# Performance work log

Measured on AMD Instinct MI355X. Metric: run time of the kernel, lower is better.

Reference implementation:

```python
import jax, jax.numpy as jnp
import numpy as np

KINEMATIC_CHAIN = [[0, 2, 5, 8, 11], [0, 1, 4, 7, 10], [0, 3, 6, 9, 12, 15],
                   [9, 14, 17, 19, 21], [9, 13, 16, 18, 20]]
PATHS = [c[1:] for c in KINEMATIC_CHAIN]  # paths = chain[1:] per gauss_integral_motion
FRAMES, JOINTS = 16384, 22


def setup_inputs() -> dict:
    key = jax.random.key(0)
    k1, k2 = jax.random.split(key)
    motion1 = jax.random.normal(k1, (FRAMES, JOINTS, 3), dtype=jnp.float32)
    motion2 = jax.random.normal(k2, (FRAMES, JOINTS, 3), dtype=jnp.float32)
    return {"motion1": motion1, "motion2": motion2}


def _safe_normalize(v):
    # vec / norm(vec) if norm != 0 else zeros  (matches the torch list comp)
    n = jnp.linalg.norm(v, axis=-1, keepdims=True)
    return jnp.where(n > 0, v / jnp.where(n > 0, n, 1.0), 0.0)


def _gli_pair(p1, p2):
    """Sum of Gauss link integrals over all segment pairs of two paths.
    p1: (L1, 3), p2: (L2, 3) -> scalar. Vectorized over the (L1-1, L2-1) segment grid."""
    s1, e1 = p1[:-1, None, :], p1[1:, None, :]   # (n1, 1, 3)
    s2, e2 = p2[None, :-1, :], p2[None, 1:, :]   # (1, n2, 3)
    r13, r14 = s2 - s1, e2 - s1
    r23, r24 = s2 - e1, e2 - e1
    r12, r34 = e1 - s1, e2 - s2
    faces = [jnp.cross(r13, r14), jnp.cross(r14, r24),
             jnp.cross(r24, r23), jnp.cross(r23, r13)]
    nf = [_safe_normalize(f) for f in faces]
    gli = jnp.zeros(jnp.broadcast_shapes(r13.shape[:-1], r24.shape[:-1]), p1.dtype)
    for i in range(4):
        d = jnp.clip(jnp.sum(nf[i] * nf[(i + 1) % 4], axis=-1), -1.0, 1.0)
        gli = gli + jnp.arcsin(d)
    sign = jnp.sum(jnp.cross(r34, r12) * r13, axis=-1)
    gli = gli * jnp.where(sign > 0, 1.0, -1.0) / (4.0 * jnp.pi)
    return jnp.sum(gli)


def _window_mask(motion1, motion2):
    # xz bounding-box overlap per frame, then dilate each contiguous run by 1
    # frame on each side (start = count-1, end = count+1-1 in the torch code).
    def bbox(m):  # (F, J, 3) -> min/max over joints of x and z
        x, z = m[..., 0], m[..., 2]
        return x.min(1), x.max(1), z.min(1), z.max(1)
    x1n, x1x, z1n, z1x = bbox(motion1)
    x2n, x2x, z2n, z2x = bbox(motion2)
    ov_x = ~((x1x < x2n) | (x2x < x1n))
    ov_z = ~((z1x < z2n) | (z2x < z1n))
    f = ov_x & ov_z  # (F,) bool
    false1 = jnp.zeros((1,), dtype=bool)
    prev = jnp.concatenate([false1, f[:-1]])
    nxt = jnp.concatenate([f[1:], false1])
    return f | prev | nxt


def _gli_motion(motion1, motion2):
    frame = motion1.shape[0]
    n_paths = len(PATHS)
    mask = _window_mask(motion1, motion2).astype(motion1.dtype)  # (F,)
    # GLI_motion[i, a, b]: vmap each path-pair over frames (25 fixed pairs)
    rows = []
    for pa in PATHS:
        p1 = motion1[:, jnp.asarray(pa), :]  # (F, La, 3)
        cols = []
        for pb in PATHS:
            p2 = motion2[:, jnp.asarray(pb), :]  # (F, Lb, 3)
            cols.append(jax.vmap(_gli_pair)(p1, p2))  # (F,)
        rows.append(jnp.stack(cols, axis=-1))  # (F, n_paths)
    gli = jnp.stack(rows, axis=-2)  # (F, n_paths, n_paths)
    gli = gli * mask[:, None, None]  # frames outside windows stay zero
    vel = jnp.abs(gli[1:] - gli[:-1]).reshape(frame - 1, n_paths * n_paths)
    return jnp.max(vel, axis=1)  # (F-1,)


def reference(motion1, motion2):
    return _gli_motion(motion1, motion2)
```

## Files before the change

kernel.cpp:

```cpp
#include <hip/hip_runtime.h>
#include <math.h>

#define NFRAMES 16384
#define NJOINTS 22
#define NPATHS  5
#define NPAIRS  (NPATHS * NPATHS)
#define NSEG    16
#define GSTRIDE 32
#define FSTR    (NJOINTS * 3)

typedef float v2f __attribute__((ext_vector_type(2)));

__constant__ int2 c_seg[NSEG] = {
    {6,15},{15,24},{24,33},
    {3,12},{12,21},{21,30},
    {9,18},{18,27},{27,36},{36,45},
    {42,51},{51,57},{57,63},
    {39,48},{48,54},{54,60}
};
__constant__ int c_pstart[NPATHS] = {0, 3, 6, 10, 13};
__constant__ int c_plen[NPATHS]   = {3, 3, 4, 3, 3};

struct V3 { v2f x, y, z; };
__device__ __forceinline__ V3 vsub(V3 a, V3 b) { V3 r; r.x=a.x-b.x; r.y=a.y-b.y; r.z=a.z-b.z; return r; }
__device__ __forceinline__ v2f vdot(V3 a, V3 b) { return a.x*b.x + a.y*b.y + a.z*b.z; }
__device__ __forceinline__ V3 vcross(V3 a, V3 b) {
    V3 r;
    r.x = a.y*b.z - a.z*b.y;
    r.y = a.z*b.x - a.x*b.z;
    r.z = a.x*b.y - a.y*b.x;
    return r;
}

__device__ __forceinline__ v2f vfast_asin(v2f x) {
    v2f a = __builtin_elementwise_max(x, -x);
    v2f p = a * -0.0187293f + 0.0742610f;
    p = a * p + -0.2121144f;
    p = a * p + 1.5707288f;
    v2f s;
    s.x = __builtin_amdgcn_sqrtf(1.0f - a.x);
    s.y = __builtin_amdgcn_sqrtf(1.0f - a.y);
    v2f r = 1.5707963268f - s * p;
    r.x = (x.x < 0.0f) ? -r.x : r.x;
    r.y = (x.y < 0.0f) ? -r.y : r.y;
    return r;
}

__device__ __forceinline__ v2f vasin_term(v2f d, v2f ma, v2f mb) {
    v2f m = ma * mb;
    v2f rs;
    rs.x = __builtin_amdgcn_rsqf(m.x);
    rs.y = __builtin_amdgcn_rsqf(m.y);
    v2f one = 1.0f, mone = -1.0f;
    v2f x = __builtin_elementwise_min(one, __builtin_elementwise_max(mone, d * rs));
    v2f r = vfast_asin(x);
    r.x = (ma.x > 0.0f && mb.x > 0.0f) ? r.x : 0.0f;
    r.y = (ma.y > 0.0f && mb.y > 0.0f) ? r.y : 0.0f;
    return r;
}

__global__ __launch_bounds__(256) void k_gli(const float* __restrict__ m1,
                                             const float* __restrict__ m2,
                                             float* __restrict__ gli,
                                             int* __restrict__ ov) {
    __shared__ v2f sA[FSTR];
    __shared__ v2f sB[FSTR];
    __shared__ float sT0[257];
    __shared__ float sT1[257];

    int f0 = blockIdx.x * 2;
    int t = threadIdx.x;
    const float* a0 = m1 + (size_t)f0 * FSTR;
    const float* b0 = m2 + (size_t)f0 * FSTR;

    float* sAf = (float*)sA;
    float* sBf = (float*)sB;
    if (t < FSTR)               sAf[2 * t] = a0[t];
    else if (t < 2 * FSTR)      sBf[2 * (t - FSTR)] = b0[t - FSTR];
    else if (t < 3 * FSTR)      sAf[2 * (t - 2 * FSTR) + 1] = a0[FSTR + (t - 2 * FSTR)];
    else                        sBf[2 * (t - 3 * FSTR) + 1] = b0[FSTR + (t - 3 * FSTR)];
    if (t < 8)                  sBf[2 * (58 + t) + 1] = b0[FSTR + 58 + t];
    if (t == 0) { sT0[256] = 0.0f; sT1[256] = 0.0f; }
    __syncthreads();

    int i = t >> 4;
    int j = t & 15;
    int2 o1 = c_seg[i];
    int2 o2 = c_seg[j];
    V3 s1; s1.x = sA[o1.x]; s1.y = sA[o1.x+1]; s1.z = sA[o1.x+2];
    V3 e1; e1.x = sA[o1.y]; e1.y = sA[o1.y+1]; e1.z = sA[o1.y+2];
    V3 s2; s2.x = sB[o2.x]; s2.y = sB[o2.x+1]; s2.z = sB[o2.x+2];
    V3 e2; e2.x = sB[o2.y]; e2.y = sB[o2.y+1]; e2.z = sB[o2.y+2];

    V3 r12 = vsub(e1, s1);
    V3 r13 = vsub(s2, s1);
    V3 r14 = vsub(e2, s1);

    V3 f0v = vcross(r13, r14);
    V3 c1  = vcross(r12, r13);
    V3 c2  = vcross(r12, r14);
    V3 f2  = vsub(vsub(c2, c1), f0v);

    v2f q0 = vdot(f0v, f0v);
    v2f q1 = vdot(c2, c2);
    v2f q2 = vdot(f2, f2);
    v2f q3 = vdot(c1, c1);

    v2f g = vasin_term( vdot(f0v, c2), q0, q1)
          + vasin_term( vdot(c2, f2),  q1, q2)
          + vasin_term(-vdot(f2, c1),  q2, q3)
          + vasin_term(-vdot(c1, f0v), q3, q0);

    v2f sg = -vdot(c2, r13);
    sT0[t] = (sg.x > 0.0f) ? g.x : -g.x;
    sT1[t] = (sg.y > 0.0f) ? g.y : -g.y;

    int w = t >> 6;
    if (w == 1 || w == 2) {
        int fr = w - 1;
        int half = (t >> 5) & 1;
        int jj = t & 31;
        if (jj > NJOINTS - 1) jj = NJOINTS - 1;
        const float* p = (half ? sBf : sAf);
        float x = p[2 * (jj * 3 + 0) + fr];
        float z = p[2 * (jj * 3 + 2) + fr];
        float xn = x, xx = x, zn = z, zx = z;
#pragma unroll
        for (int k = 1; k < 32; k <<= 1) {
            xn = fminf(xn, __shfl_xor(xn, k, 32));
            xx = fmaxf(xx, __shfl_xor(xx, k, 32));
            zn = fminf(zn, __shfl_xor(zn, k, 32));
            zx = fmaxf(zx, __shfl_xor(zx, k, 32));
        }
        float oxn = __shfl_xor(xn, 32, 64);
        float oxx = __shfl_xor(xx, 32, 64);
        float ozn = __shfl_xor(zn, 32, 64);
        float ozx = __shfl_xor(zx, 32, 64);
        if ((t & 63) == 0) {
            bool ovx = !((xx < oxn) || (oxx < xn));
            bool ovz = !((zx < ozn) || (ozx < zn));
            ov[f0 + fr] = (ovx && ovz) ? 1 : 0;
        }
    }
    __syncthreads();

    int tt = -1;
    const float* sT = sT0;
    int fo = f0;
    if (t < NPAIRS) { tt = t; }
    else if (t >= 32 && t < 32 + NPAIRS) { tt = t - 32; sT = sT1; fo = f0 + 1; }
    if (tt >= 0) {
        int pa = (tt * 205) >> 10;
        int pb = tt - pa * 5;
        int ia0 = c_pstart[pa], na = c_plen[pa];
        int ib0 = c_pstart[pb], nb = c_plen[pb];
        float s = 0.0f;
#pragma unroll
        for (int ka = 0; ka < 4; ka++) {
#pragma unroll
            for (int kb = 0; kb < 4; kb++) {
                int idx = (ka < na && kb < nb) ? ((ia0 + ka) * 16 + (ib0 + kb)) : 256;
                s += sT[idx];
            }
        }
        gli[(size_t)fo * GSTRIDE + tt] = s * 0.07957747154594767f;
    }
}

__global__ void k_out(const float* __restrict__ gli, const int* __restrict__ ov,
                      float* __restrict__ out) {
    int f = blockIdx.x * blockDim.x + threadIdx.x;
    if (f >= NFRAMES - 1) return;

    int m0 = ov[f];
    if (f > 0) m0 |= ov[f - 1];
    m0 |= ov[f + 1];

    int m1 = ov[f + 1] | ov[f];
    if (f + 2 <= NFRAMES - 1) m1 |= ov[f + 2];

    float ma = m0 ? 1.0f : 0.0f;
    float mb = m1 ? 1.0f : 0.0f;

    const float4* g0v = (const float4*)(gli + (size_t)f * GSTRIDE);
    const float4* g1v = (const float4*)(gli + (size_t)(f + 1) * GSTRIDE);
    float v = 0.0f;
#pragma unroll
    for (int q = 0; q < 6; q++) {
        float4 u0 = g0v[q];
        float4 u1 = g1v[q];
        v = fmaxf(v, fabsf(u1.x * mb - u0.x * ma));
        v = fmaxf(v, fabsf(u1.y * mb - u0.y * ma));
        v = fmaxf(v, fabsf(u1.z * mb - u0.z * ma));
        v = fmaxf(v, fabsf(u1.w * mb - u0.w * ma));
    }
    {
        float u0 = ((const float*)g0v)[24];
        float u1 = ((const float*)g1v)[24];
        v = fmaxf(v, fabsf(u1 * mb - u0 * ma));
    }
    out[f] = v;
}

extern "C" void kernel_launch(void* const* d_in, const int* in_sizes, int n_in,
                              void* d_out, int out_size, void* d_ws, size_t ws_size,
                              hipStream_t stream) {
    const float* m1 = (const float*)d_in[0];
    const float* m2 = (const float*)d_in[1];
    float* out = (float*)d_out;

    float* gli = (float*)d_ws;
    int* ov = (int*)(gli + (size_t)NFRAMES * GSTRIDE);

    k_gli<<<NFRAMES / 2, 256, 0, stream>>>(m1, m2, gli, ov);

    {
        int threads = 256;
        int blocks = (NFRAMES - 1 + threads - 1) / threads;
        k_out<<<blocks, threads, 0, stream>>>(gli, ov, out);
    }
}
```

Baseline: 80.69 us.

## Give each wavefront its own frame pair, processing 8 frames per block

Restructures k_gli so each of the four wavefronts in a block handles a separate frame pair. Each lane loops over 4 segment pairs, reusing its second-path segment loads across the loop, and every wavefront also does its own bbox overlap reduction using paired (v2f) shuffles. This cuts the block count by four and keeps lanes busy that previously sat idle in the bbox and reduction phases. The cost is more serial work per thread and more shared memory per block, which could lower occupancy or hurt latency hiding. The __syncthreads calls remain block-wide even though the data is now per-wavefront.

```diff
diff --git a/kernel.cpp b/kernel.cpp
--- a/kernel.cpp
+++ b/kernel.cpp
@@ -8,6 +8,7 @@
 #define NSEG    16
 #define GSTRIDE 32
 #define FSTR    (NJOINTS * 3)
+#define FPB     8
 
 typedef float v2f __attribute__((ext_vector_type(2)));
 
@@ -59,111 +60,140 @@
     return r;
 }
 
+__device__ __forceinline__ v2f shfl_xor_v2(v2f v, int mask, int width) {
+    v2f r;
+    r.x = __shfl_xor(v.x, mask, width);
+    r.y = __shfl_xor(v.y, mask, width);
+    return r;
+}
+
 __global__ __launch_bounds__(256) void k_gli(const float* __restrict__ m1,
                                              const float* __restrict__ m2,
                                              float* __restrict__ gli,
                                              int* __restrict__ ov) {
-    __shared__ v2f sA[FSTR];
-    __shared__ v2f sB[FSTR];
-    __shared__ float sT0[257];
-    __shared__ float sT1[257];
-
-    int f0 = blockIdx.x * 2;
+    __shared__ v2f sF[4][2 * FSTR];
+    __shared__ v2f sT[4][260];
+
     int t = threadIdx.x;
-    const float* a0 = m1 + (size_t)f0 * FSTR;
-    const float* b0 = m2 + (size_t)f0 * FSTR;
-
-    float* sAf = (float*)sA;
-    float* sBf = (float*)sB;
-    if (t < FSTR)               sAf[2 * t] = a0[t];
-    else if (t < 2 * FSTR)      sBf[2 * (t - FSTR)] = b0[t - FSTR];
-    else if (t < 3 * FSTR)      sAf[2 * (t - 2 * FSTR) + 1] = a0[FSTR + (t - 2 * FSTR)];
-    else                        sBf[2 * (t - 3 * FSTR) + 1] = b0[FSTR + (t - 3 * FSTR)];
-    if (t < 8)                  sBf[2 * (58 + t) + 1] = b0[FSTR + 58 + t];
-    if (t == 0) { sT0[256] = 0.0f; sT1[256] = 0.0f; }
+    int w = t >> 6;
+    int l = t & 63;
+    int fp = blockIdx.x * FPB + 2 * w;
+    const float* a = m1 + (size_t)fp * FSTR;
+    const float* b = m2 + (size_t)fp * FSTR;
+
+    v2f* sFw = sF[w];
+    float* sFf = (float*)sFw;
+
+    {
+        int u1 = l + 64;
+        int fr1 = (u1 >= FSTR) ? 1 : 0;
+        int co1 = u1 - fr1 * FSTR;
+        float a0v = a[l], a1v = a[u1];
+        float b0v = b[l], b1v = b[u1];
+        sFf[2 * l] = a0v;
+        sFf[2 * co1 + fr1] = a1v;
+        sFf[2 * FSTR + 2 * l] = b0v;
+        sFf[2 * FSTR + 2 * co1 + fr1] = b1v;
+        if (l < 2 * FSTR - 128) {
+            int u2 = l + 128;
+            int co2 = u2 - FSTR;
+            sFf[2 * co2 + 1] = a[u2];
+            sFf[2 * FSTR + 2 * co2 + 1] = b[u2];
+        }
+        if (l == 32) sT[w][256] = v2f{0.0f, 0.0f};
+    }
     __syncthreads();
 
-    int i = t >> 4;
-    int j = t & 15;
-    int2 o1 = c_seg[i];
-    int2 o2 = c_seg[j];
-    V3 s1; s1.x = sA[o1.x]; s1.y = sA[o1.x+1]; s1.z = sA[o1.x+2];
-    V3 e1; e1.x = sA[o1.y]; e1.y = sA[o1.y+1]; e1.z = sA[o1.y+2];
-    V3 s2; s2.x = sB[o2.x]; s2.y = sB[o2.x+1]; s2.z = sB[o2.x+2];
-    V3 e2; e2.x = sB[o2.y]; e2.y = sB[o2.y+1]; e2.z = sB[o2.y+2];
-
-    V3 r12 = vsub(e1, s1);
-    V3 r13 = vsub(s2, s1);
-    V3 r14 = vsub(e2, s1);
-
-    V3 f0v = vcross(r13, r14);
-    V3 c1  = vcross(r12, r13);
-    V3 c2  = vcross(r12, r14);
-    V3 f2  = vsub(vsub(c2, c1), f0v);
-
-    v2f q0 = vdot(f0v, f0v);
-    v2f q1 = vdot(c2, c2);
-    v2f q2 = vdot(f2, f2);
-    v2f q3 = vdot(c1, c1);
-
-    v2f g = vasin_term( vdot(f0v, c2), q0, q1)
-          + vasin_term( vdot(c2, f2),  q1, q2)
-          + vasin_term(-vdot(f2, c1),  q2, q3)
-          + vasin_term(-vdot(c1, f0v), q3, q0);
-
-    v2f sg = -vdot(c2, r13);
-    sT0[t] = (sg.x > 0.0f) ? g.x : -g.x;
-    sT1[t] = (sg.y > 0.0f) ? g.y : -g.y;
-
-    int w = t >> 6;
-    if (w == 1 || w == 2) {
-        int fr = w - 1;
-        int half = (t >> 5) & 1;
-        int jj = t & 31;
+    {
+        int j = l & 15;
+        int i0 = l >> 4;
+        int2 o2 = c_seg[j];
+        const v2f* B = sFw + FSTR;
+        V3 s2; s2.x = B[o2.x]; s2.y = B[o2.x+1]; s2.z = B[o2.x+2];
+        V3 e2; e2.x = B[o2.y]; e2.y = B[o2.y+1]; e2.z = B[o2.y+2];
+        V3 r34 = vsub(e2, s2);
+        for (int k = 0; k < 4; k++) {
+            int2 o1 = c_seg[i0 + 4 * k];
+            V3 s1; s1.x = sFw[o1.x]; s1.y = sFw[o1.x+1]; s1.z = sFw[o1.x+2];
+            V3 e1; e1.x = sFw[o1.y]; e1.y = sFw[o1.y+1]; e1.z = sFw[o1.y+2];
+
+            V3 r12 = vsub(e1, s1);
+            V3 r13 = vsub(s2, s1);
+            V3 r14 = vsub(e2, s1);
+
+            V3 f0v = vcross(r13, r14);
+            V3 c1  = vcross(r12, r13);
+            V3 c2  = vcross(r12, r14);
+            V3 f2  = vsub(vsub(c2, c1), f0v);
+
+            v2f q0 = vdot(f0v, f0v);
+            v2f q1 = vdot(c2, c2);
+            v2f q2 = vdot(f2, f2);
+            v2f q3 = vdot(c1, c1);
+
+            v2f g = vasin_term( vdot(f0v, c2), q0, q1)
+                  + vasin_term( vdot(c2, f2),  q1, q2)
+                  + vasin_term(-vdot(f2, c1),  q2, q3)
+                  + vasin_term(-vdot(c1, f0v), q3, q0);
+
+            v2f sg = -vdot(c2, r13);
+            v2f res;
+            res.x = (sg.x > 0.0f) ? g.x : -g.x;
+            res.y = (sg.y > 0.0f) ? g.y : -g.y;
+            sT[w][l + 64 * k] = res;
+        }
+        (void)r34;
+    }
+
+    {
+        int half = l >> 5;
+        int jj = l & 31;
         if (jj > NJOINTS - 1) jj = NJOINTS - 1;
-        const float* p = (half ? sBf : sAf);
-        float x = p[2 * (jj * 3 + 0) + fr];
-        float z = p[2 * (jj * 3 + 2) + fr];
-        float xn = x, xx = x, zn = z, zx = z;
+        const v2f* p = sFw + half * FSTR;
+        v2f x = p[jj * 3 + 0];
+        v2f z = p[jj * 3 + 2];
+        v2f xn = x, xx = x, zn = z, zx = z;
 #pragma unroll
         for (int k = 1; k < 32; k <<= 1) {
-            xn = fminf(xn, __shfl_xor(xn, k, 32));
-            xx = fmaxf(xx, __shfl_xor(xx, k, 32));
-            zn = fminf(zn, __shfl_xor(zn, k, 32));
-            zx = fmaxf(zx, __shfl_xor(zx, k, 32));
-        }
-        float oxn = __shfl_xor(xn, 32, 64);
-        float oxx = __shfl_xor(xx, 32, 64);
-        float ozn = __shfl_xor(zn, 32, 64);
-        float ozx = __shfl_xor(zx, 32, 64);
-        if ((t & 63) == 0) {
-            bool ovx = !((xx < oxn) || (oxx < xn));
-            bool ovz = !((zx < ozn) || (ozx < zn));
-            ov[f0 + fr] = (ovx && ovz) ? 1 : 0;
+            xn = __builtin_elementwise_min(xn, shfl_xor_v2(xn, k, 32));
+            xx = __builtin_elementwise_max(xx, shfl_xor_v2(xx, k, 32));
+            zn = __builtin_elementwise_min(zn, shfl_xor_v2(zn, k, 32));
+            zx = __builtin_elementwise_max(zx, shfl_xor_v2(zx, k, 32));
+        }
+        v2f oxn = shfl_xor_v2(xn, 32, 64);
+        v2f oxx = shfl_xor_v2(xx, 32, 64);
+        v2f ozn = shfl_xor_v2(zn, 32, 64);
+        v2f ozx = shfl_xor_v2(zx, 32, 64);
+        if (l == 0) {
+            int2 o;
+            bool vx0 = !((xx.x < oxn.x) || (oxx.x < xn.x));
+            bool vz0 = !((zx.x < ozn.x) || (ozx.x < zn.x));
+            bool vx1 = !((xx.y < oxn.y) || (oxx.y < xn.y));
+            bool vz1 = !((zx.y < ozn.y) || (ozx.y < zn.y));
+            o.x = (vx0 && vz0) ? 1 : 0;
+            o.y = (vx1 && vz1) ? 1 : 0;
+            *(int2*)(ov + fp) = o;
         }
     }
     __syncthreads();
 
-    int tt = -1;
-    const float* sT = sT0;
-    int fo = f0;
-    if (t < NPAIRS) { tt = t; }
-    else if (t >= 32 && t < 32 + NPAIRS) { tt = t - 32; sT = sT1; fo = f0 + 1; }
-    if (tt >= 0) {
-        int pa = (tt * 205) >> 10;
-        int pb = tt - pa * 5;
+    if (l < NPAIRS) {
+        int pa = (l * 205) >> 10;
+        int pb = l - pa * 5;
         int ia0 = c_pstart[pa], na = c_plen[pa];
         int ib0 = c_pstart[pb], nb = c_plen[pb];
-        float s = 0.0f;
+        v2f s = v2f{0.0f, 0.0f};
 #pragma unroll
         for (int ka = 0; ka < 4; ka++) {
 #pragma unroll
             for (int kb = 0; kb < 4; kb++) {
                 int idx = (ka < na && kb < nb) ? ((ia0 + ka) * 16 + (ib0 + kb)) : 256;
-                s += sT[idx];
+                s += sT[w][idx];
             }
         }
-        gli[(size_t)fo * GSTRIDE + tt] = s * 0.07957747154594767f;
+        s *= 0.07957747154594767f;
+        gli[(size_t)fp * GSTRIDE + l] = s.x;
+        gli[(size_t)(fp + 1) * GSTRIDE + l] = s.y;
     }
 }
 
@@ -212,7 +242,7 @@
     float* gli = (float*)d_ws;
     int* ov = (int*)(gli + (size_t)NFRAMES * GSTRIDE);
 
-    k_gli<<<NFRAMES / 2, 256, 0, stream>>>(m1, m2, gli, ov);
+    k_gli<<<NFRAMES / FPB, 256, 0, stream>>>(m1, m2, gli, ov);
 
     {
         int threads = 256;
```

After: 79.47 us. No clear change (-1.5%).
